# Kernel tuning notes

Measured on AMD Instinct MI355X. Metric: run time of the kernel, lower is better.

Reference implementation:

```python
import jax, jax.numpy as jnp
import numpy as np
from jax import lax

N, CI, CO, K, H, W_SP, M = 32, 256, 256, 3, 64, 64, 4
TAU = 1.0 / 30.0
PAD = 1  # spatial-preserving for k=3, stride=1, dilation=1


def setup_inputs() -> dict:
    key = jax.random.key(0)
    ks = jax.random.split(key, 6)
    # kaiming_normal fan_out for the kernel bank: fan_out = CO*K*K (per torch semantics on this 6D tensor layout)
    fan_out = CO * K * K
    std = np.sqrt(2.0 / fan_out)
    x = jax.random.normal(ks[0], (N, CI, H, W_SP), dtype=jnp.float32)
    Wbank = jax.random.normal(ks[1], (CO, M, CI, K, K), dtype=jnp.float32) * std
    Bbank = jnp.zeros((CO, M), dtype=jnp.float32)
    hid = CI // M  # att_fc hidden = in_channels // num_weights
    w1 = jax.random.normal(ks[2], (hid, CI), dtype=jnp.float32) * np.sqrt(1.0 / CI)
    b1 = jnp.zeros((hid,), dtype=jnp.float32)
    w2 = jax.random.normal(ks[3], (M, hid), dtype=jnp.float32) * np.sqrt(1.0 / hid)
    b2 = jnp.zeros((M,), dtype=jnp.float32)
    return {"x": x, "Wbank": Wbank, "Bbank": Bbank, "w1": w1, "b1": b1, "w2": w2, "b2": b2}


def reference(x, Wbank, Bbank, w1, b1, w2, b2):
    n, ci, h, w = x.shape
    co = Wbank.shape[0]
    # attention over kernels: global avg pool -> 1x1 conv MLP -> softmax(logits * tau)
    pooled = jnp.mean(x, axis=(2, 3))                      # N,Ci
    hmid = jax.nn.relu(pooled @ w1.T + b1)                 # N,hid
    logits = hmid @ w2.T + b2                              # N,M
    pi = jax.nn.softmax(logits * TAU, axis=1)              # N,M
    # per-sample aggregated kernels and biases
    wn = jnp.einsum("nm,omikl->noikl", pi, Wbank)          # N,Co,Ci,K,K
    bn = pi @ Bbank.T                                      # N,Co
    # batch-as-groups conv2d (spatial-preserving)
    xg = x.reshape(1, n * ci, h, w)
    wg = wn.reshape(n * co, ci, K, K)
    y = lax.conv_general_dilated(
        xg, wg,
        window_strides=(1, 1),
        padding=[(PAD, PAD), (PAD, PAD)],
        rhs_dilation=(1, 1),
        dimension_numbers=("NCHW", "OIHW", "NCHW"),
        feature_group_count=n,
    )
    y = y.reshape(n, co, h, w) + bn[:, :, None, None]
    return y
```

## Files before the change

### kernel.cpp

```cpp
#include <hip/hip_runtime.h>
#include <hip/hip_bf16.h>
#include <stdint.h>

typedef __bf16 bf16;
typedef __bf16 bf16x8 __attribute__((ext_vector_type(8)));
typedef float f32x4 __attribute__((ext_vector_type(4)));

#define TAU (1.0f/30.0f)

#define NB 32
#define CI 256
#define CO 256
#define HH 64
#define WW 64
#define HID 64

#define WN_ELEMS ((size_t)NB*8*9*16*512)
#define WN_BYTES (WN_ELEMS*2)
#define XB_ELEMS ((size_t)NB*32*64*64*8)
#define XB_BYTES (XB_ELEMS*2)

__device__ __forceinline__ void async16(void* lds_uniform_base, const void* g_perlane) {
  __builtin_amdgcn_global_load_lds(
      (const __attribute__((address_space(1))) uint32_t*)g_perlane,
      (__attribute__((address_space(3))) uint32_t*)lds_uniform_base, 16, 0, 0);
}

__global__ void cvt_pool_kernel(const float* __restrict__ x, bf16* __restrict__ xb,
                                float* __restrict__ pooled) {
  const int cg = blockIdx.x, n = blockIdx.y, tid = threadIdx.x;
  const float* base = x + ((size_t)n*CI + cg*8)*4096;
  bf16* ob = xb + ((size_t)n*32 + cg)*4096*8;
  float s[8];
#pragma unroll
  for (int j = 0; j < 8; ++j) s[j] = 0.f;
  for (int it = 0; it < 16; ++it) {
    int pos = it*256 + tid;
    bf16x8 o;
#pragma unroll
    for (int j = 0; j < 8; ++j) {
      float v = base[(size_t)j*4096 + pos];
      s[j] += v;
      o[j] = (bf16)v;
    }
    *(bf16x8*)(ob + (size_t)pos*8) = o;
  }
  __shared__ float red[4][8];
#pragma unroll
  for (int j = 0; j < 8; ++j)
#pragma unroll
    for (int off = 32; off; off >>= 1) s[j] += __shfl_xor(s[j], off);
  int wv = tid >> 6, lane = tid & 63;
  if (lane == 0)
#pragma unroll
    for (int j = 0; j < 8; ++j) red[wv][j] = s[j];
  __syncthreads();
  if (tid < 8) {
    float t = red[0][tid] + red[1][tid] + red[2][tid] + red[3][tid];
    pooled[n*CI + cg*8 + tid] = t * (1.0f/4096.0f);
  }
}

__global__ void attn_kernel(const float* __restrict__ pooled,
                            const float* __restrict__ w1, const float* __restrict__ b1,
                            const float* __restrict__ w2, const float* __restrict__ b2,
                            float* __restrict__ pi) {
  int n = blockIdx.x, h = threadIdx.x;
  __shared__ float hm[HID];
  __shared__ float lgs[4];
  const float* pr = pooled + n*CI;
  float s = b1[h];
  for (int c = 0; c < CI; ++c) s += pr[c] * w1[h*CI + c];
  hm[h] = s > 0.f ? s : 0.f;
  __syncthreads();
  if (h < 4) {
    float lg = b2[h];
    for (int k = 0; k < HID; ++k) lg += hm[k] * w2[h*HID + k];
    lgs[h] = lg * TAU;
  }
  __syncthreads();
  if (h == 0) {
    float mx = fmaxf(fmaxf(lgs[0], lgs[1]), fmaxf(lgs[2], lgs[3]));
    float e0 = expf(lgs[0]-mx), e1 = expf(lgs[1]-mx), e2 = expf(lgs[2]-mx), e3 = expf(lgs[3]-mx);
    float inv = 1.f / (e0+e1+e2+e3);
    pi[n*4+0] = e0*inv; pi[n*4+1] = e1*inv; pi[n*4+2] = e2*inv; pi[n*4+3] = e3*inv;
  }
}

__global__ void agg_kernel(const float* __restrict__ Wbank, const float* __restrict__ pi,
                           bf16* __restrict__ wn) {
  int wid = blockIdx.x * 4 + (threadIdx.x >> 6);
  int lane = threadIdx.x & 63;
  int c = wid / 144;
  int rem = wid - c*144;
  int kk = rem >> 4;
  int cbg = rem & 15;
  int co  = cbg*16 + (lane & 15);
  int ci0 = c*32 + (lane >> 4)*8;
  float w[4][8];
#pragma unroll
  for (int m = 0; m < 4; ++m)
#pragma unroll
    for (int j = 0; j < 8; ++j)
      w[m][j] = Wbank[(size_t)((co*4 + m)*256 + ci0 + j)*9 + kk];
  for (int n = 0; n < NB; ++n) {
    float p0 = pi[n*4+0], p1 = pi[n*4+1], p2 = pi[n*4+2], p3 = pi[n*4+3];
    bf16x8 o;
#pragma unroll
    for (int j = 0; j < 8; ++j)
      o[j] = (bf16)(p0*w[0][j] + p1*w[1][j] + p2*w[2][j] + p3*w[3][j]);
    *(bf16x8*)(wn + ((size_t)n*1152 + c*144 + kk*16 + cbg)*512 + lane*8) = o;
  }
}

#define XROWS 10
#define XW 66
#define XS_E (4*XROWS*XW*8)
#define WA_E (9*4*512)

__global__ __launch_bounds__(256, 1)
void conv_kernel(const bf16* __restrict__ xb, const bf16* __restrict__ wn,
                 const float* __restrict__ pi, const float* __restrict__ Bbank,
                 float* __restrict__ y) {
  __shared__ __align__(16) bf16 xs[2][XS_E];
  __shared__ __align__(16) bf16 wa[2][WA_E];
  __shared__ float bns[64];
  const int tid = threadIdx.x;
  const int wv = tid >> 6, lane = tid & 63;
  const int l = lane & 15, u = lane >> 4;
  const int flat = blockIdx.x;
  const int wid = ((flat & 7) << 7) + (flat >> 3);
  const int n   = wid >> 5;
  const int hwb = (wid >> 2) & 7;
  const int cot = wid & 3;
  const int h0 = hwb * 8;

  for (int i = tid; i < 2*XS_E/8; i += 256) ((int4*)xs)[i] = int4{0,0,0,0};
  if (tid < 64) {
    int co = cot*64 + tid;
    bns[tid] = pi[n*4+0]*Bbank[co*4+0] + pi[n*4+1]*Bbank[co*4+1]
             + pi[n*4+2]*Bbank[co*4+2] + pi[n*4+3]*Bbank[co*4+3];
  }

  f32x4 acc[2][4][4];
#pragma unroll
  for (int o = 0; o < 2; ++o)
#pragma unroll
    for (int a = 0; a < 4; ++a)
#pragma unroll
      for (int b = 0; b < 4; ++b)
#pragma unroll
        for (int k = 0; k < 4; ++k) acc[o][a][b][k] = 0.f;

  const bf16* wnb = wn + (size_t)n * 1152 * 512;
  const bf16* xgb = xb + (size_t)n*32*4096*8 + lane*8;

  auto STAGE = [&](int c, int b) {
    const bf16* seg = wnb + (size_t)c*144*512 + (size_t)(cot*4 + wv)*512 + lane*8;
#pragma unroll
    for (int kk = 0; kk < 9; ++kk)
      async16(&wa[b][kk*2048 + wv*512], seg + (size_t)kk*16*512);
    const bf16* xg = xgb + (size_t)(c*4 + wv)*4096*8;
#pragma unroll
    for (int r = 0; r < XROWS; ++r) {
      int hp = h0 - 1 + r;
      if (hp >= 0 && hp < HH)
        async16(&xs[b][((wv*XROWS + r)*XW + 1)*8], xg + (size_t)hp*64*8);
    }
  };

  __syncthreads();
  STAGE(0, 0);

  for (int c = 0; c < 8; ++c) {
    __syncthreads();
    if (c < 7) STAGE(c + 1, (c + 1) & 1);
    const bf16* xsb = xs[c & 1];
    const bf16* wab = wa[c & 1];
#pragma unroll
    for (int kx = 0; kx < 3; ++kx) {
      bf16x8 bfr[4][4];
#pragma unroll
      for (int rr = 0; rr < 4; ++rr)
#pragma unroll
        for (int f = 0; f < 4; ++f)
          bfr[rr][f] = *(const bf16x8*)(&xsb[((u*XROWS + wv*2 + rr)*XW + f*16 + l + kx)*8]);
#pragma unroll
      for (int ky = 0; ky < 3; ++ky) {
        const int kk = ky*3 + kx;
#pragma unroll
        for (int cb = 0; cb < 4; ++cb) {
          bf16x8 afr = *(const bf16x8*)(&wab[kk*2048 + cb*512 + lane*8]);
#pragma unroll
          for (int o = 0; o < 2; ++o)
#pragma unroll
            for (int f = 0; f < 4; ++f)
              acc[o][cb][f] = __builtin_amdgcn_mfma_f32_16x16x32_bf16(afr, bfr[o+ky][f], acc[o][cb][f], 0, 0, 0);
        }
      }
    }
  }
#pragma unroll
  for (int o = 0; o < 2; ++o) {
    const int h = h0 + wv*2 + o;
#pragma unroll
    for (int cb = 0; cb < 4; ++cb) {
#pragma unroll
      for (int f = 0; f < 4; ++f) {
        const int wcol = f*16 + l;
#pragma unroll
        for (int r4 = 0; r4 < 4; ++r4) {
          const int col = cb*16 + u*4 + r4;
          y[(((size_t)n*CO + cot*64 + col)*HH + h)*WW + wcol] = acc[o][cb][f][r4] + bns[col];
        }
      }
    }
  }
}

extern "C" void kernel_launch(void* const* d_in, const int* in_sizes, int n_in,
                              void* d_out, int out_size, void* d_ws, size_t ws_size,
                              hipStream_t stream) {
  const float* x     = (const float*)d_in[0];
  const float* Wbank = (const float*)d_in[1];
  const float* Bbank = (const float*)d_in[2];
  const float* w1    = (const float*)d_in[3];
  const float* b1    = (const float*)d_in[4];
  const float* w2    = (const float*)d_in[5];
  const float* b2    = (const float*)d_in[6];
  float* y = (float*)d_out;

  bf16*  wn     = (bf16*)d_ws;
  bf16*  xb     = (bf16*)((char*)d_ws + WN_BYTES);
  float* pooled = (float*)((char*)d_ws + WN_BYTES + XB_BYTES);
  float* pi     = pooled + NB*CI;

  dim3 cg(32, NB);
  cvt_pool_kernel<<<cg, 256, 0, stream>>>(x, xb, pooled);
  attn_kernel<<<NB, HID, 0, stream>>>(pooled, w1, b1, w2, b2, pi);
  agg_kernel<<<288, 256, 0, stream>>>(Wbank, pi, wn);
  conv_kernel<<<1024, 256, 0, stream>>>(xb, wn, pi, Bbank, y);
}
```

Measured before the change: 223.7 us.

## Single-buffer conv input tile and load weights directly from global

Removes the double-buffered LDS staging of both activation and weight tiles. Activations are now single-buffered with an extra barrier per channel chunk, and the weight fragments are read straight from global memory into registers. The launch bound is raised to allow two blocks per CU. The aim is to cut LDS footprint so occupancy can double and overlap comes from multiple resident blocks. The cost is losing the async prefetch overlap and taking global-latency weight loads inside the MFMA loop.

```diff
diff --git a/kernel.cpp b/kernel.cpp
--- a/kernel.cpp
+++ b/kernel.cpp
@@ -116,14 +116,12 @@
 #define XROWS 10
 #define XW 66
 #define XS_E (4*XROWS*XW*8)
-#define WA_E (9*4*512)
-
-__global__ __launch_bounds__(256, 1)
+
+__global__ __launch_bounds__(256, 2)
 void conv_kernel(const bf16* __restrict__ xb, const bf16* __restrict__ wn,
                  const float* __restrict__ pi, const float* __restrict__ Bbank,
                  float* __restrict__ y) {
-  __shared__ __align__(16) bf16 xs[2][XS_E];
-  __shared__ __align__(16) bf16 wa[2][WA_E];
+  __shared__ __align__(16) bf16 xs[XS_E];
   __shared__ float bns[64];
   const int tid = threadIdx.x;
   const int wv = tid >> 6, lane = tid & 63;
@@ -135,7 +133,7 @@
   const int cot = wid & 3;
   const int h0 = hwb * 8;
 
-  for (int i = tid; i < 2*XS_E/8; i += 256) ((int4*)xs)[i] = int4{0,0,0,0};
+  for (int i = tid; i < XS_E/8; i += 256) ((int4*)xs)[i] = int4{0,0,0,0};
   if (tid < 64) {
     int co = cot*64 + tid;
     bns[tid] = pi[n*4+0]*Bbank[co*4+0] + pi[n*4+1]*Bbank[co*4+1]
@@ -152,31 +150,22 @@
 #pragma unroll
         for (int k = 0; k < 4; ++k) acc[o][a][b][k] = 0.f;
 
-  const bf16* wnb = wn + (size_t)n * 1152 * 512;
+  const bf16* wnb = wn + (size_t)n * 1152 * 512 + (size_t)cot*4*512 + lane*8;
   const bf16* xgb = xb + (size_t)n*32*4096*8 + lane*8;
-
-  auto STAGE = [&](int c, int b) {
-    const bf16* seg = wnb + (size_t)c*144*512 + (size_t)(cot*4 + wv)*512 + lane*8;
-#pragma unroll
-    for (int kk = 0; kk < 9; ++kk)
-      async16(&wa[b][kk*2048 + wv*512], seg + (size_t)kk*16*512);
-    const bf16* xg = xgb + (size_t)(c*4 + wv)*4096*8;
-#pragma unroll
-    for (int r = 0; r < XROWS; ++r) {
-      int hp = h0 - 1 + r;
-      if (hp >= 0 && hp < HH)
-        async16(&xs[b][((wv*XROWS + r)*XW + 1)*8], xg + (size_t)hp*64*8);
-    }
-  };
-
-  __syncthreads();
-  STAGE(0, 0);
 
   for (int c = 0; c < 8; ++c) {
     __syncthreads();
-    if (c < 7) STAGE(c + 1, (c + 1) & 1);
-    const bf16* xsb = xs[c & 1];
-    const bf16* wab = wa[c & 1];
+    {
+      const bf16* xg = xgb + (size_t)(c*4 + wv)*4096*8;
+#pragma unroll
+      for (int r = 0; r < XROWS; ++r) {
+        int hp = h0 - 1 + r;
+        if (hp >= 0 && hp < HH)
+          async16(&xs[((wv*XROWS + r)*XW + 1)*8], xg + (size_t)hp*64*8);
+      }
+    }
+    __syncthreads();
+    const bf16* wc = wnb + (size_t)c*144*512;
 #pragma unroll
     for (int kx = 0; kx < 3; ++kx) {
       bf16x8 bfr[4][4];
@@ -184,19 +173,21 @@
       for (int rr = 0; rr < 4; ++rr)
 #pragma unroll
         for (int f = 0; f < 4; ++f)
-          bfr[rr][f] = *(const bf16x8*)(&xsb[((u*XROWS + wv*2 + rr)*XW + f*16 + l + kx)*8]);
+          bfr[rr][f] = *(const bf16x8*)(&xs[((u*XROWS + wv*2 + rr)*XW + f*16 + l + kx)*8]);
 #pragma unroll
       for (int ky = 0; ky < 3; ++ky) {
         const int kk = ky*3 + kx;
-#pragma unroll
-        for (int cb = 0; cb < 4; ++cb) {
-          bf16x8 afr = *(const bf16x8*)(&wab[kk*2048 + cb*512 + lane*8]);
+        bf16x8 afr[4];
+#pragma unroll
+        for (int cb = 0; cb < 4; ++cb)
+          afr[cb] = *(const bf16x8*)(wc + (size_t)(kk*16 + cb)*512);
+#pragma unroll
+        for (int cb = 0; cb < 4; ++cb)
 #pragma unroll
           for (int o = 0; o < 2; ++o)
 #pragma unroll
             for (int f = 0; f < 4; ++f)
-              acc[o][cb][f] = __builtin_amdgcn_mfma_f32_16x16x32_bf16(afr, bfr[o+ky][f], acc[o][cb][f], 0, 0, 0);
-        }
+              acc[o][cb][f] = __builtin_amdgcn_mfma_f32_16x16x32_bf16(afr[cb], bfr[o+ky][f], acc[o][cb][f], 0, 0, 0);
       }
     }
   }
```

After: 199.3 us. 1.12x faster.
